# Kernel tuning notes

Measured on AMD Instinct MI355X. Metric: run time of the kernel, lower is better.

The kernel has to match this reference:

```python
import jax, jax.numpy as jnp
import numpy as np

N, T, D_FEAT, H = 8192, 60, 6, 64
NEG_SLOPE = 0.01  # torch LeakyReLU default


def setup_inputs() -> dict:
    key = jax.random.key(0)
    ks = jax.random.split(key, 20)
    s = lambda k, shape, fan: jax.random.normal(k, shape, jnp.float32) * (1.0 / np.sqrt(fan))
    inp = {
        'x': jax.random.normal(ks[0], (N, T, D_FEAT), jnp.float32),
        # LSTM layer 0 (input D_FEAT) and layer 1 (input H); gate order i,f,g,o
        'Wih0': s(ks[1], (4 * H, D_FEAT), H), 'Whh0': s(ks[2], (4 * H, H), H),
        'bih0': s(ks[3], (4 * H,), H), 'bhh0': s(ks[4], (4 * H,), H),
        'Wih1': s(ks[5], (4 * H, H), H), 'Whh1': s(ks[6], (4 * H, H), H),
        'bih1': s(ks[7], (4 * H,), H), 'bhh1': s(ks[8], (4 * H,), H),
        # GAT layer: transformation Linear(H,H) and attention vector a [2H,1] (randn in torch)
        'Wt': s(ks[9], (H, H), H), 'bt': s(ks[10], (H,), H),
        'a': jax.random.normal(ks[11], (2 * H, 1), jnp.float32),
        # fc and fc_out
        'Wfc': s(ks[12], (H, H), H), 'bfc': s(ks[13], (H,), H),
        'Wout': s(ks[14], (1, H), H), 'bout': s(ks[15], (1,), H),
    }
    return inp


def _lstm_layer(x, Wih, Whh, bih, bhh):
    # x: [N, T, Din] -> outputs [N, T, H]
    xg = jnp.einsum('ntd,gd->ntg', x, Wih) + bih + bhh  # precompute input gates

    def step(carry, xt):
        h, c = carry
        gates = xt + h @ Whh.T  # [N, 4H]
        i, f, g, o = jnp.split(gates, 4, axis=-1)
        c = jax.nn.sigmoid(f) * c + jax.nn.sigmoid(i) * jnp.tanh(g)
        h = jax.nn.sigmoid(o) * jnp.tanh(c)
        return (h, c), h

    n = x.shape[0]
    h0 = jnp.zeros((n, Whh.shape[1]), x.dtype)
    (_, _), hs = jax.lax.scan(step, (h0, h0), jnp.swapaxes(xg, 0, 1))
    return jnp.swapaxes(hs, 0, 1)


def _gat_layer(x, Wt, bt, a):
    # att[i,j] = leaky_relu(a1 . Wx_j + a2 . Wx_i); softmax over j; out = att @ x
    h = x @ Wt.T + bt                    # [N, H]
    hdim = h.shape[1]
    s1 = (h @ a[:hdim]).squeeze(-1)      # a1 . Wx_j  -> column term
    s2 = (h @ a[hdim:]).squeeze(-1)      # a2 . Wx_i  -> row term
    scores = jax.nn.leaky_relu(s2[:, None] + s1[None, :], NEG_SLOPE)  # [N, N]
    att = jax.nn.softmax(scores, axis=1)
    return att @ x


def reference(x, Wih0, Whh0, bih0, bhh0, Wih1, Whh1, bih1, bhh1,
              Wt, bt, a, Wfc, bfc, Wout, bout):
    out = _lstm_layer(x, Wih0, Whh0, bih0, bhh0)
    out = _lstm_layer(out, Wih1, Whh1, bih1, bhh1)
    last = out[:, -1, :]                 # [N, H]
    hidden = _gat_layer(last, Wt, bt, a) + last  # num_layers_gat = 1
    hidden = jax.nn.leaky_relu(hidden @ Wfc.T + bfc, NEG_SLOPE)
    return (hidden @ Wout.T + bout).squeeze(-1)  # [N]
```

## Files before the change

kernel.cpp:

```cpp
#include <hip/hip_runtime.h>

#define NN 8192
#define TT 60
#define DF 6
#define HH 64
#define GG 256
#define RS 132
#define CH 32
#define NCH (NN / CH)

typedef _Float16 half8 __attribute__((ext_vector_type(8)));
typedef float f32x4 __attribute__((ext_vector_type(4)));
#define MFMA16(a, b, c) __builtin_amdgcn_mfma_f32_16x16x32_f16((a), (b), (c), 0, 0, 0)

__device__ __forceinline__ float sigmoidf_(float x) {
    return __builtin_amdgcn_rcpf(1.0f + __expf(-x));
}
__device__ __forceinline__ float tanhf_(float x) {
    return __builtin_fmaf(2.0f, __builtin_amdgcn_rcpf(1.0f + __expf(-2.0f * x)), -1.0f);
}
__device__ __forceinline__ float lrelu_(float x) { return x > 0.0f ? x : 0.01f * x; }

__device__ __forceinline__ half8 ldw8(const float* __restrict__ p) {
    const float4* q = (const float4*)p;
    float4 u = q[0], v = q[1];
    half8 r;
    r[0]=(_Float16)u.x; r[1]=(_Float16)u.y; r[2]=(_Float16)u.z; r[3]=(_Float16)u.w;
    r[4]=(_Float16)v.x; r[5]=(_Float16)v.y; r[6]=(_Float16)v.z; r[7]=(_Float16)v.w;
    return r;
}

#define SXW (TT * 8 + 8)

__global__ __launch_bounds__(512, 4)
void lstm_fused_kernel(const float* __restrict__ x,
                       const float* __restrict__ Wih0, const float* __restrict__ Whh0,
                       const float* __restrict__ bih0, const float* __restrict__ bhh0,
                       const float* __restrict__ Wih1, const float* __restrict__ Whh1,
                       const float* __restrict__ bih1, const float* __restrict__ bhh1,
                       float* __restrict__ last_out)
{
    __shared__ _Float16 sxp[16][SXW];
    __shared__ _Float16 h0buf[2][16][72];
    __shared__ _Float16 h1buf[2][16][72];
    __shared__ _Float16 zero16[8];

    const int tid  = threadIdx.x;
    const int w    = tid >> 6;
    const int grp  = w >> 2;
    const int cg   = w & 3;
    const int lane = tid & 63;
    const int quad = lane >> 4;
    const int l15  = lane & 15;
    const int hc   = cg * 16 + l15;
    const int n0   = blockIdx.x * 16;

    for (int i = tid; i < 16 * SXW / 2; i += 512) ((unsigned*)sxp)[i] = 0u;
    for (int i = tid; i < 2 * 16 * 72 / 2; i += 512) ((unsigned*)h0buf)[i] = 0u;
    for (int i = tid; i < 2 * 16 * 72 / 2; i += 512) ((unsigned*)h1buf)[i] = 0u;
    if (tid < 4) ((unsigned*)zero16)[tid] = 0u;
    __syncthreads();

    for (int idx = tid; idx < 16 * TT * DF; idx += 512) {
        const int m = idx / (TT * DF);
        const int r = idx - m * (TT * DF);
        const int t = r / DF;
        const int d = r - t * DF;
        sxp[m][t * 8 + d] = (_Float16)x[(size_t)(n0 + m) * (TT * DF) + r];
    }

    half8 wA[4][2], wB[4][2];
    float bias[4];
    half8 hzero;
    #pragma unroll
    for (int j = 0; j < 8; j++) hzero[j] = (_Float16)0.f;

    if (grp == 0) {
        #pragma unroll
        for (int nt = 0; nt < 4; nt++) {
            const int g = nt * 64 + hc;
            wA[nt][0] = ldw8(Whh0 + (size_t)g * HH + quad * 8);
            wA[nt][1] = ldw8(Whh0 + (size_t)g * HH + 32 + quad * 8);
            bias[nt]  = bih0[g] + bhh0[g];
            half8 t = hzero;
            if (quad == 0) {
                #pragma unroll
                for (int j = 0; j < DF; j++) t[j] = (_Float16)Wih0[g * DF + j];
            }
            wB[nt][0] = t;
            wB[nt][1] = hzero;
        }
    } else {
        #pragma unroll
        for (int nt = 0; nt < 4; nt++) {
            const int g = nt * 64 + hc;
            wA[nt][0] = ldw8(Wih1 + (size_t)g * HH + quad * 8);
            wA[nt][1] = ldw8(Wih1 + (size_t)g * HH + 32 + quad * 8);
            wB[nt][0] = ldw8(Whh1 + (size_t)g * HH + quad * 8);
            wB[nt][1] = ldw8(Whh1 + (size_t)g * HH + 32 + quad * 8);
            bias[nt]  = bih1[g] + bhh1[g];
        }
    }

    float cs[4] = {0.f, 0.f, 0.f, 0.f};
    __syncthreads();

    for (int i = 0; i <= TT; i++) {
        const int p = i & 1;
        if (grp == 0) {
            if (i < TT) {
                const half8 a0 = *(const half8*)&h0buf[p][l15][quad * 8];
                const half8 a1 = *(const half8*)&h0buf[p][l15][32 + quad * 8];
                const _Float16* xap = (quad == 0) ? &sxp[l15][i * 8] : zero16;
                const half8 ax = *(const half8*)xap;
                f32x4 gv[4];
                #pragma unroll
                for (int nt = 0; nt < 4; nt++) {
                    f32x4 c; c[0] = bias[nt]; c[1] = bias[nt]; c[2] = bias[nt]; c[3] = bias[nt];
                    c = MFMA16(ax, wB[nt][0], c);
                    c = MFMA16(a0, wA[nt][0], c);
                    c = MFMA16(a1, wA[nt][1], c);
                    gv[nt] = c;
                }
                _Float16 (*h0w)[72] = h0buf[p ^ 1];
                #pragma unroll
                for (int reg = 0; reg < 4; reg++) {
                    const float gi = gv[0][reg], gf = gv[1][reg], gc = gv[2][reg], go = gv[3][reg];
                    const float cc = sigmoidf_(gf) * cs[reg] + sigmoidf_(gi) * tanhf_(gc);
                    cs[reg] = cc;
                    h0w[quad * 4 + reg][hc] = (_Float16)(sigmoidf_(go) * tanhf_(cc));
                }
            }
        } else {
            if (i > 0) {
                const half8 a00 = *(const half8*)&h0buf[p][l15][quad * 8];
                const half8 a01 = *(const half8*)&h0buf[p][l15][32 + quad * 8];
                const half8 a10 = *(const half8*)&h1buf[p][l15][quad * 8];
                const half8 a11 = *(const half8*)&h1buf[p][l15][32 + quad * 8];
                f32x4 gv[4];
                #pragma unroll
                for (int nt = 0; nt < 4; nt++) {
                    f32x4 c; c[0] = bias[nt]; c[1] = bias[nt]; c[2] = bias[nt]; c[3] = bias[nt];
                    c = MFMA16(a00, wA[nt][0], c);
                    c = MFMA16(a01, wA[nt][1], c);
                    c = MFMA16(a10, wB[nt][0], c);
                    c = MFMA16(a11, wB[nt][1], c);
                    gv[nt] = c;
                }
                _Float16 (*h1w)[72] = h1buf[p ^ 1];
                #pragma unroll
                for (int reg = 0; reg < 4; reg++) {
                    const float gi = gv[0][reg], gf = gv[1][reg], gc = gv[2][reg], go = gv[3][reg];
                    const float cc = sigmoidf_(gf) * cs[reg] + sigmoidf_(gi) * tanhf_(gc);
                    cs[reg] = cc;
                    const float hv = sigmoidf_(go) * tanhf_(cc);
                    h1w[quad * 4 + reg][hc] = (_Float16)hv;
                    if (i == TT) last_out[(size_t)(n0 + quad * 4 + reg) * HH + hc] = hv;
                }
            }
        }
        __syncthreads();
    }
}

__global__ void gat_prep_kernel(const float* __restrict__ last,
                                const float* __restrict__ Wt, const float* __restrict__ bt,
                                const float* __restrict__ a,
                                float* __restrict__ s1, float* __restrict__ s2,
                                float* __restrict__ blkmax)
{
    __shared__ float sWtT[HH][HH + 1];
    __shared__ float slast[16][HH];
    __shared__ float sbt[HH], sa1[HH], sa2[HH];
    __shared__ float swm[4];
    const int tid = threadIdx.x;
    for (int idx = tid; idx < HH * HH; idx += 256) {
        const int h = idx >> 6, d = idx & 63;
        sWtT[d][h] = Wt[idx];
    }
    if (tid < HH) { sbt[tid] = bt[tid]; sa1[tid] = a[tid]; sa2[tid] = a[HH + tid]; }
    const int n0 = blockIdx.x * 16;
    for (int idx = tid; idx < 16 * HH; idx += 256)
        (&slast[0][0])[idx] = last[(size_t)n0 * HH + idx];
    __syncthreads();
    const int w = tid >> 6, l = tid & 63;
    float wmax = -1e30f;
    for (int rr = 0; rr < 4; rr++) {
        const int r = w * 4 + rr;
        float acc = sbt[l];
        #pragma unroll
        for (int d = 0; d < HH; d++) acc += slast[r][d] * sWtT[d][l];
        float p1 = acc * sa1[l], p2 = acc * sa2[l];
        #pragma unroll
        for (int off = 32; off > 0; off >>= 1) {
            p1 += __shfl_xor(p1, off);
            p2 += __shfl_xor(p2, off);
        }
        if (l == 0) { s1[n0 + r] = p1; s2[n0 + r] = p2; }
        wmax = fmaxf(wmax, p1);
    }
    if (l == 0) swm[w] = wmax;
    __syncthreads();
    if (tid == 0) blkmax[blockIdx.x] = fmaxf(fmaxf(swm[0], swm[1]), fmaxf(swm[2], swm[3]));
}

__global__ void gat_finalize_kernel(const float* __restrict__ s1, const float* __restrict__ s2,
                                    const float* __restrict__ blkmax,
                                    float* __restrict__ Z, float* __restrict__ Ai, float* __restrict__ Bi,
                                    float* __restrict__ Dj, float* __restrict__ Uj, float* __restrict__ Wj,
                                    int* __restrict__ rank)
{
    __shared__ float red[256];
    const int tid = threadIdx.x;
    red[tid] = fmaxf(blkmax[tid], blkmax[tid + 256]);
    __syncthreads();
    for (int s = 128; s > 0; s >>= 1) {
        if (tid < s) red[tid] = fmaxf(red[tid], red[tid + s]);
        __syncthreads();
    }
    const float s1max = red[0];
    for (int i = blockIdx.x * 256 + tid; i < NN; i += 256 * 32) {
        const float z  = s2[i] + s1max;
        const float mi = lrelu_(z);
        Z[i]  = z;
        Ai[i] = __expf(z - mi);
        Bi[i] = __expf(0.01f * z - mi);
        const float d = s1[i] - s1max;
        Dj[i] = d;
        Uj[i] = __expf(d);
        Wj[i] = __expf(0.01f * d);
        rank[i] = 0;
    }
}

__global__ __launch_bounds__(256)
void rank_kernel(const float* __restrict__ Dj, int* __restrict__ rank)
{
    __shared__ float sd[1024];
    const int tid = threadIdx.x;
    const int j   = blockIdx.x * 256 + tid;
    const float dj = Dj[j];
    const int kbase = blockIdx.y * 1024;
    for (int i = tid; i < 1024; i += 256) sd[i] = Dj[kbase + i];
    __syncthreads();
    int cnt = 0;
    #pragma unroll 4
    for (int q = 0; q < 256; q++) {
        const float4 dk = ((const float4*)sd)[q];
        const int k0 = kbase + q * 4;
        cnt += (dk.x < dj || (dk.x == dj && k0     < j)) ? 1 : 0;
        cnt += (dk.y < dj || (dk.y == dj && k0 + 1 < j)) ? 1 : 0;
        cnt += (dk.z < dj || (dk.z == dj && k0 + 2 < j)) ? 1 : 0;
        cnt += (dk.w < dj || (dk.w == dj && k0 + 3 < j)) ? 1 : 0;
    }
    atomicAdd(&rank[j], cnt);
}

__global__ __launch_bounds__(256)
void scatter_kernel(const float* __restrict__ last,
                    const float* __restrict__ Dj, const float* __restrict__ Uj,
                    const float* __restrict__ Wj, const int* __restrict__ rank,
                    float* __restrict__ sortedRow, float* __restrict__ sortedD)
{
    const int tid = threadIdx.x;
    const int wv = tid >> 6, lane = tid & 63;
    #pragma unroll
    for (int it = 0; it < 8; it++) {
        const int j = blockIdx.x * 32 + wv * 8 + it;
        const int r = rank[j];
        const float u = Uj[j], w = Wj[j];
        const float lv = last[(size_t)j * HH + lane];
        float* row = sortedRow + (size_t)r * RS;
        row[lane]      = u * lv;
        row[64 + lane] = w * lv;
        if (lane == 0) {
            row[128] = u;
            row[129] = w;
            sortedD[r] = Dj[j];
        }
    }
}

__global__ __launch_bounds__(256)
void scanA_kernel(const float* __restrict__ sortedRow, float* __restrict__ chunkSum)
{
    const int c = threadIdx.x;
    if (c >= 130) return;
    const int b = blockIdx.x;
    const float* base = sortedRow + (size_t)b * CH * RS + c;
    float s = 0.f;
    #pragma unroll 8
    for (int r = 0; r < CH; r++) s += base[(size_t)r * RS];
    chunkSum[b * RS + c] = s;
}

__global__ __launch_bounds__(256)
void scanC_kernel(const float* __restrict__ sortedRow, const float* __restrict__ chunkSum,
                  float* __restrict__ PP)
{
    const int c = threadIdx.x;
    if (c >= 130) return;
    const int b = blockIdx.x;
    const bool rev = (c < 64) || (c == 128);
    float run = 0.f;
    #pragma unroll 8
    for (int bb = 0; bb < NCH; bb++) {
        const float v = chunkSum[bb * RS + c];
        const bool take = rev ? (bb > b) : (bb < b);
        run += take ? v : 0.f;
    }
    if (rev) {
        if (b == NCH - 1) PP[(size_t)NN * RS + c] = 0.f;
        #pragma unroll 4
        for (int r = CH - 1; r >= 0; r--) {
            const size_t t = (size_t)b * CH + r;
            run += sortedRow[t * RS + c];
            PP[t * RS + c] = run;
        }
    } else {
        #pragma unroll 4
        for (int r = 0; r < CH; r++) {
            const size_t t = (size_t)b * CH + r;
            PP[t * RS + c] = run;
            run += sortedRow[t * RS + c];
        }
        if (b == NCH - 1) PP[(size_t)NN * RS + c] = run;
    }
}

__global__ __launch_bounds__(256)
void applyfc_kernel(const float* __restrict__ last,
                    const float* __restrict__ Z, const float* __restrict__ Ai, const float* __restrict__ Bi,
                    const float* __restrict__ sortedD, const float* __restrict__ PP,
                    const float* __restrict__ Wfc, const float* __restrict__ bfc,
                    const float* __restrict__ Wout, const float* __restrict__ bout,
                    float* __restrict__ out)
{
    __shared__ float sdD[NN];
    __shared__ float sW[HH][HH + 1];
    __shared__ float sb[HH], sa[HH];
    const int tid = threadIdx.x;
    for (int idx = tid; idx < NN; idx += 256) sdD[idx] = sortedD[idx];
    for (int idx = tid; idx < HH * HH; idx += 256) {
        const int h = idx >> 6, d = idx & 63;
        sW[d][h] = Wfc[idx];
    }
    if (tid < HH) { sb[tid] = bfc[tid]; sa[tid] = Wout[tid]; }
    __syncthreads();

    const int wv = tid >> 6, lane = tid & 63;
    const int base_i = (blockIdx.x * 4 + wv) * 8;
    const float bo = bout[0];
    for (int batch = 0; batch < 2; batch++) {
        const int i0 = base_i + batch * 4;
        float zi[4]; int lo[4], hi[4];
        #pragma unroll
        for (int q = 0; q < 4; q++) { zi[q] = Z[i0 + q]; lo[q] = 0; hi[q] = NN; }
        for (int iter = 0; iter < 13; iter++) {
            #pragma unroll
            for (int q = 0; q < 4; q++) {
                if (lo[q] < hi[q]) {
                    const int mid = (lo[q] + hi[q]) >> 1;
                    const float dm = sdD[mid];
                    if (zi[q] + dm > 0.f) hi[q] = mid; else lo[q] = mid + 1;
                }
            }
        }
        #pragma unroll
        for (int q = 0; q < 4; q++) {
            const int i = i0 + q;
            const int t = lo[q];
            const float ai = Ai[i], bi = Bi[i];
            const float* row = PP + (size_t)t * RS;
            const float pu  = row[lane];
            const float pw  = row[64 + lane];
            const float pud = row[128];
            const float pwd = row[129];
            const float numer = bi * pw + ai * pu;
            const float den   = bi * pwd + ai * pud;
            const float lv = last[(size_t)i * HH + lane];
            const float gv = numer * __builtin_amdgcn_rcpf(den) + lv;
            float acc = sb[lane];
            #pragma unroll
            for (int d = 0; d < HH; d++) acc += __shfl(gv, d) * sW[d][lane];
            float prod = lrelu_(acc) * sa[lane];
            #pragma unroll
            for (int off = 32; off > 0; off >>= 1) prod += __shfl_xor(prod, off);
            if (lane == 0) out[i] = prod + bo;
        }
    }
}

extern "C" void kernel_launch(void* const* d_in, const int* in_sizes, int n_in,
                              void* d_out, int out_size, void* d_ws, size_t ws_size,
                              hipStream_t stream)
{
    (void)in_sizes; (void)n_in; (void)out_size; (void)ws_size;
    const float* x    = (const float*)d_in[0];
    const float* Wih0 = (const float*)d_in[1];
    const float* Whh0 = (const float*)d_in[2];
    const float* bih0 = (const float*)d_in[3];
    const float* bhh0 = (const float*)d_in[4];
    const float* Wih1 = (const float*)d_in[5];
    const float* Whh1 = (const float*)d_in[6];
    const float* bih1 = (const float*)d_in[7];
    const float* bhh1 = (const float*)d_in[8];
    const float* Wt   = (const float*)d_in[9];
    const float* bt   = (const float*)d_in[10];
    const float* a    = (const float*)d_in[11];
    const float* Wfc  = (const float*)d_in[12];
    const float* bfc  = (const float*)d_in[13];
    const float* Wout = (const float*)d_in[14];
    const float* bout = (const float*)d_in[15];
    float* out = (float*)d_out;

    float* ws        = (float*)d_ws;
    float* last      = ws;
    float* s1        = last + (size_t)NN*HH;
    float* s2        = s1 + NN;
    float* Z         = s2 + NN;
    float* Ai        = Z + NN;
    float* Bi        = Ai + NN;
    float* Dj        = Bi + NN;
    float* Uj        = Dj + NN;
    float* Wj        = Uj + NN;
    float* blkmax    = Wj + NN;
    int*   rank      = (int*)(blkmax + 512);
    float* sortedD   = (float*)(rank + NN);
    float* sortedRow = sortedD + NN;
    float* PP        = sortedRow + (size_t)NN*RS;
    float* chunkSum  = PP + (size_t)(NN+1)*RS;

    lstm_fused_kernel<<<dim3(NN / 16), dim3(512), 0, stream>>>(
        x, Wih0, Whh0, bih0, bhh0, Wih1, Whh1, bih1, bhh1, last);
    gat_prep_kernel<<<dim3(NN / 16), dim3(256), 0, stream>>>(
        last, Wt, bt, a, s1, s2, blkmax);
    gat_finalize_kernel<<<dim3(32), dim3(256), 0, stream>>>(
        s1, s2, blkmax, Z, Ai, Bi, Dj, Uj, Wj, rank);
    rank_kernel<<<dim3(NN / 256, 8), dim3(256), 0, stream>>>(Dj, rank);
    scatter_kernel<<<dim3(NN / 32), dim3(256), 0, stream>>>(
        last, Dj, Uj, Wj, rank, sortedRow, sortedD);
    scanA_kernel<<<dim3(NCH), dim3(256), 0, stream>>>(sortedRow, chunkSum);
    scanC_kernel<<<dim3(NCH), dim3(256), 0, stream>>>(sortedRow, chunkSum, PP);
    applyfc_kernel<<<dim3(NN / 32), dim3(256), 0, stream>>>(
        last, Z, Ai, Bi, sortedD, PP, Wfc, bfc, Wout, bout, out);
}
```

Baseline: 287.1 us.

## Fuse GAT tail kernels into one persistent kernel with software grid barriers

Replaces the seven GAT/FC kernels with a single 256-block persistent kernel that separates phases with atomic-counter grid barriers. This removes per-launch overhead and inter-kernel gaps. It also folds Wt into the attention vector (a^T Wt), so s1/s2 come from a dot product instead of a full 64x64 transform, and keeps per-row values in shared memory instead of global. The cost is that all 256 blocks must be co-resident for the barriers to avoid deadlock, and the rank counting now runs in fewer blocks doing more serial work each.

```diff
diff --git a/kernel.cpp b/kernel.cpp
--- a/kernel.cpp
+++ b/kernel.cpp
@@ -7,7 +7,7 @@
 #define GG 256
 #define RS 132
 #define CH 32
-#define NCH (NN / CH)
+#define NB 256
 
 typedef _Float16 half8 __attribute__((ext_vector_type(8)));
 typedef float f32x4 __attribute__((ext_vector_type(4)));
@@ -163,231 +163,229 @@
     }
 }
 
-__global__ void gat_prep_kernel(const float* __restrict__ last,
-                                const float* __restrict__ Wt, const float* __restrict__ bt,
-                                const float* __restrict__ a,
-                                float* __restrict__ s1, float* __restrict__ s2,
-                                float* __restrict__ blkmax)
+__global__ void bar_init_kernel(int* bar) {
+    if (threadIdx.x == 0) { bar[0] = 0; bar[1] = 0; }
+}
+
+__device__ __forceinline__ void gridbar(int* __restrict__ bar) {
+    __syncthreads();
+    if (threadIdx.x == 0) {
+        int* cnt = bar;
+        int* gen = bar + 1;
+        const int g = atomicAdd(gen, 0);
+        __threadfence();
+        if (atomicAdd(cnt, 1) == NB - 1) {
+            atomicExch(cnt, 0);
+            __threadfence();
+            atomicAdd(gen, 1);
+        } else {
+            while (atomicAdd(gen, 0) == g) __builtin_amdgcn_s_sleep(8);
+        }
+        __threadfence();
+    }
+    __syncthreads();
+}
+
+__global__ __launch_bounds__(256, 1)
+void gat_tail_kernel(const float* __restrict__ last,
+                     const float* __restrict__ Wt, const float* __restrict__ bt,
+                     const float* __restrict__ a,
+                     const float* __restrict__ Wfc, const float* __restrict__ bfc,
+                     const float* __restrict__ Wout, const float* __restrict__ bout,
+                     float* __restrict__ blkmax, float* __restrict__ Dj,
+                     float* __restrict__ sortedRow, float* __restrict__ sortedD,
+                     float* __restrict__ chunkSum, float* __restrict__ PP,
+                     int* __restrict__ bar,
+                     float* __restrict__ out)
 {
-    __shared__ float sWtT[HH][HH + 1];
-    __shared__ float slast[16][HH];
-    __shared__ float sbt[HH], sa1[HH], sa2[HH];
-    __shared__ float swm[4];
-    const int tid = threadIdx.x;
+    __shared__ float big[NN];
+    __shared__ float sWfc[HH][HH + 1];
+    __shared__ float sv1[HH], sv2[HH], sbF[HH], saF[HH];
+    __shared__ float sc12[2];
+    __shared__ float sS1[32], sS2[32], sZ[32], sAi[32], sBi[32], sU[32], sWw[32], sD[32];
+    __shared__ int   sRank[32];
+    __shared__ float sred[256];
+
+    const int tid  = threadIdx.x;
+    const int b    = blockIdx.x;
+    const int j0   = b * 32;
+    const int wv   = tid >> 6;
+    const int lane = tid & 63;
+
     for (int idx = tid; idx < HH * HH; idx += 256) {
         const int h = idx >> 6, d = idx & 63;
-        sWtT[d][h] = Wt[idx];
-    }
-    if (tid < HH) { sbt[tid] = bt[tid]; sa1[tid] = a[tid]; sa2[tid] = a[HH + tid]; }
-    const int n0 = blockIdx.x * 16;
-    for (int idx = tid; idx < 16 * HH; idx += 256)
-        (&slast[0][0])[idx] = last[(size_t)n0 * HH + idx];
-    __syncthreads();
-    const int w = tid >> 6, l = tid & 63;
-    float wmax = -1e30f;
-    for (int rr = 0; rr < 4; rr++) {
-        const int r = w * 4 + rr;
-        float acc = sbt[l];
-        #pragma unroll
-        for (int d = 0; d < HH; d++) acc += slast[r][d] * sWtT[d][l];
-        float p1 = acc * sa1[l], p2 = acc * sa2[l];
+        sWfc[d][h] = Wfc[idx];
+    }
+    if (tid < HH) {
+        float a1 = 0.f, a2 = 0.f;
+        #pragma unroll 8
+        for (int h = 0; h < HH; h++) {
+            const float wt = Wt[h * HH + tid];
+            a1 += wt * a[h];
+            a2 += wt * a[HH + h];
+        }
+        sv1[tid] = a1; sv2[tid] = a2;
+    } else if (tid == 64 || tid == 65) {
+        const float* av = a + (tid - 64) * HH;
+        float c = 0.f;
+        #pragma unroll 8
+        for (int h = 0; h < HH; h++) c += bt[h] * av[h];
+        sc12[tid - 64] = c;
+    } else if (tid >= 128 && tid < 192) {
+        sbF[tid - 128] = bfc[tid - 128];
+    } else if (tid >= 192) {
+        saF[tid - 192] = Wout[tid - 192];
+    }
+    __syncthreads();
+
+    #pragma unroll
+    for (int jj = 0; jj < 8; jj++) {
+        const int jl = wv * 8 + jj;
+        const float lv = last[(size_t)(j0 + jl) * HH + lane];
+        float p1 = lv * sv1[lane];
+        float p2 = lv * sv2[lane];
         #pragma unroll
         for (int off = 32; off > 0; off >>= 1) {
             p1 += __shfl_xor(p1, off);
             p2 += __shfl_xor(p2, off);
         }
-        if (l == 0) { s1[n0 + r] = p1; s2[n0 + r] = p2; }
-        wmax = fmaxf(wmax, p1);
-    }
-    if (l == 0) swm[w] = wmax;
-    __syncthreads();
-    if (tid == 0) blkmax[blockIdx.x] = fmaxf(fmaxf(swm[0], swm[1]), fmaxf(swm[2], swm[3]));
-}
-
-__global__ void gat_finalize_kernel(const float* __restrict__ s1, const float* __restrict__ s2,
-                                    const float* __restrict__ blkmax,
-                                    float* __restrict__ Z, float* __restrict__ Ai, float* __restrict__ Bi,
-                                    float* __restrict__ Dj, float* __restrict__ Uj, float* __restrict__ Wj,
-                                    int* __restrict__ rank)
-{
-    __shared__ float red[256];
-    const int tid = threadIdx.x;
-    red[tid] = fmaxf(blkmax[tid], blkmax[tid + 256]);
+        if (lane == 0) { sS1[jl] = p1 + sc12[0]; sS2[jl] = p2 + sc12[1]; }
+    }
+    __syncthreads();
+    if (tid < 32) {
+        float m = sS1[tid];
+        #pragma unroll
+        for (int off = 16; off > 0; off >>= 1) m = fmaxf(m, __shfl_xor(m, off));
+        if (tid == 0) blkmax[b] = m;
+    }
+    gridbar(bar);
+
+    sred[tid] = blkmax[tid];
     __syncthreads();
     for (int s = 128; s > 0; s >>= 1) {
-        if (tid < s) red[tid] = fmaxf(red[tid], red[tid + s]);
+        if (tid < s) sred[tid] = fmaxf(sred[tid], sred[tid + s]);
         __syncthreads();
     }
-    const float s1max = red[0];
-    for (int i = blockIdx.x * 256 + tid; i < NN; i += 256 * 32) {
-        const float z  = s2[i] + s1max;
+    const float s1max = sred[0];
+    if (tid < 32) {
+        const float z  = sS2[tid] + s1max;
         const float mi = lrelu_(z);
-        Z[i]  = z;
-        Ai[i] = __expf(z - mi);
-        Bi[i] = __expf(0.01f * z - mi);
-        const float d = s1[i] - s1max;
-        Dj[i] = d;
-        Uj[i] = __expf(d);
-        Wj[i] = __expf(0.01f * d);
-        rank[i] = 0;
-    }
-}
-
-__global__ __launch_bounds__(256)
-void rank_kernel(const float* __restrict__ Dj, int* __restrict__ rank)
-{
-    __shared__ float sd[1024];
-    const int tid = threadIdx.x;
-    const int j   = blockIdx.x * 256 + tid;
-    const float dj = Dj[j];
-    const int kbase = blockIdx.y * 1024;
-    for (int i = tid; i < 1024; i += 256) sd[i] = Dj[kbase + i];
-    __syncthreads();
-    int cnt = 0;
-    #pragma unroll 4
-    for (int q = 0; q < 256; q++) {
-        const float4 dk = ((const float4*)sd)[q];
-        const int k0 = kbase + q * 4;
-        cnt += (dk.x < dj || (dk.x == dj && k0     < j)) ? 1 : 0;
-        cnt += (dk.y < dj || (dk.y == dj && k0 + 1 < j)) ? 1 : 0;
-        cnt += (dk.z < dj || (dk.z == dj && k0 + 2 < j)) ? 1 : 0;
-        cnt += (dk.w < dj || (dk.w == dj && k0 + 3 < j)) ? 1 : 0;
-    }
-    atomicAdd(&rank[j], cnt);
-}
-
-__global__ __launch_bounds__(256)
-void scatter_kernel(const float* __restrict__ last,
-                    const float* __restrict__ Dj, const float* __restrict__ Uj,
-                    const float* __restrict__ Wj, const int* __restrict__ rank,
-                    float* __restrict__ sortedRow, float* __restrict__ sortedD)
-{
-    const int tid = threadIdx.x;
-    const int wv = tid >> 6, lane = tid & 63;
+        sZ[tid]  = z;
+        sAi[tid] = __expf(z - mi);
+        sBi[tid] = __expf(0.01f * z - mi);
+        const float d = sS1[tid] - s1max;
+        sD[tid] = d;
+        Dj[j0 + tid] = d;
+        sU[tid]  = __expf(d);
+        sWw[tid] = __expf(0.01f * d);
+        sRank[tid] = 0;
+    }
+    gridbar(bar);
+
+    for (int idx = tid; idx < NN; idx += 256) big[idx] = Dj[idx];
+    __syncthreads();
+    {
+        const int jl = tid & 31;
+        const int part = tid >> 5;
+        const float dj = sD[jl];
+        const int jglob = j0 + jl;
+        int cnt = 0;
+        const int k0 = part * (NN / 8);
+        #pragma unroll 4
+        for (int k = k0; k < k0 + NN / 8; k++) {
+            const float dk = big[k];
+            cnt += (dk < dj || (dk == dj && k < jglob)) ? 1 : 0;
+        }
+        atomicAdd(&sRank[jl], cnt);
+    }
+    __syncthreads();
     #pragma unroll
-    for (int it = 0; it < 8; it++) {
-        const int j = blockIdx.x * 32 + wv * 8 + it;
-        const int r = rank[j];
-        const float u = Uj[j], w = Wj[j];
-        const float lv = last[(size_t)j * HH + lane];
+    for (int jj = 0; jj < 8; jj++) {
+        const int jl = wv * 8 + jj;
+        const int r = sRank[jl];
+        const float u = sU[jl], w = sWw[jl];
+        const float lv = last[(size_t)(j0 + jl) * HH + lane];
         float* row = sortedRow + (size_t)r * RS;
         row[lane]      = u * lv;
         row[64 + lane] = w * lv;
         if (lane == 0) {
             row[128] = u;
             row[129] = w;
-            sortedD[r] = Dj[j];
-        }
-    }
-}
-
-__global__ __launch_bounds__(256)
-void scanA_kernel(const float* __restrict__ sortedRow, float* __restrict__ chunkSum)
-{
-    const int c = threadIdx.x;
-    if (c >= 130) return;
-    const int b = blockIdx.x;
-    const float* base = sortedRow + (size_t)b * CH * RS + c;
-    float s = 0.f;
-    #pragma unroll 8
-    for (int r = 0; r < CH; r++) s += base[(size_t)r * RS];
-    chunkSum[b * RS + c] = s;
-}
-
-__global__ __launch_bounds__(256)
-void scanC_kernel(const float* __restrict__ sortedRow, const float* __restrict__ chunkSum,
-                  float* __restrict__ PP)
-{
-    const int c = threadIdx.x;
-    if (c >= 130) return;
-    const int b = blockIdx.x;
-    const bool rev = (c < 64) || (c == 128);
-    float run = 0.f;
-    #pragma unroll 8
-    for (int bb = 0; bb < NCH; bb++) {
-        const float v = chunkSum[bb * RS + c];
-        const bool take = rev ? (bb > b) : (bb < b);
-        run += take ? v : 0.f;
-    }
-    if (rev) {
-        if (b == NCH - 1) PP[(size_t)NN * RS + c] = 0.f;
-        #pragma unroll 4
-        for (int r = CH - 1; r >= 0; r--) {
-            const size_t t = (size_t)b * CH + r;
-            run += sortedRow[t * RS + c];
-            PP[t * RS + c] = run;
-        }
-    } else {
-        #pragma unroll 4
-        for (int r = 0; r < CH; r++) {
-            const size_t t = (size_t)b * CH + r;
-            PP[t * RS + c] = run;
-            run += sortedRow[t * RS + c];
-        }
-        if (b == NCH - 1) PP[(size_t)NN * RS + c] = run;
-    }
-}
-
-__global__ __launch_bounds__(256)
-void applyfc_kernel(const float* __restrict__ last,
-                    const float* __restrict__ Z, const float* __restrict__ Ai, const float* __restrict__ Bi,
-                    const float* __restrict__ sortedD, const float* __restrict__ PP,
-                    const float* __restrict__ Wfc, const float* __restrict__ bfc,
-                    const float* __restrict__ Wout, const float* __restrict__ bout,
-                    float* __restrict__ out)
-{
-    __shared__ float sdD[NN];
-    __shared__ float sW[HH][HH + 1];
-    __shared__ float sb[HH], sa[HH];
-    const int tid = threadIdx.x;
-    for (int idx = tid; idx < NN; idx += 256) sdD[idx] = sortedD[idx];
-    for (int idx = tid; idx < HH * HH; idx += 256) {
-        const int h = idx >> 6, d = idx & 63;
-        sW[d][h] = Wfc[idx];
-    }
-    if (tid < HH) { sb[tid] = bfc[tid]; sa[tid] = Wout[tid]; }
-    __syncthreads();
-
-    const int wv = tid >> 6, lane = tid & 63;
-    const int base_i = (blockIdx.x * 4 + wv) * 8;
+            sortedD[r] = sD[jl];
+        }
+    }
+    gridbar(bar);
+
+    if (tid < 130) {
+        const float* base = sortedRow + (size_t)b * CH * RS + tid;
+        float s = 0.f;
+        #pragma unroll 8
+        for (int r = 0; r < CH; r++) s += base[(size_t)r * RS];
+        chunkSum[b * RS + tid] = s;
+    }
+    gridbar(bar);
+
+    if (tid < 130) {
+        const int c = tid;
+        const bool rev = (c < 64) || (c == 128);
+        float run = 0.f;
+        #pragma unroll 8
+        for (int bb = 0; bb < NB; bb++) {
+            const float v = chunkSum[bb * RS + c];
+            run += ((rev ? (bb > b) : (bb < b)) ? v : 0.f);
+        }
+        if (rev) {
+            if (b == NB - 1) PP[(size_t)NN * RS + c] = 0.f;
+            #pragma unroll 4
+            for (int r = CH - 1; r >= 0; r--) {
+                const size_t t = (size_t)b * CH + r;
+                run += sortedRow[t * RS + c];
+                PP[t * RS + c] = run;
+            }
+        } else {
+            #pragma unroll 4
+            for (int r = 0; r < CH; r++) {
+                const size_t t = (size_t)b * CH + r;
+                PP[t * RS + c] = run;
+                run += sortedRow[t * RS + c];
+            }
+            if (b == NB - 1) PP[(size_t)NN * RS + c] = run;
+        }
+    }
+    gridbar(bar);
+
+    for (int idx = tid; idx < NN; idx += 256) big[idx] = sortedD[idx];
+    __syncthreads();
     const float bo = bout[0];
-    for (int batch = 0; batch < 2; batch++) {
-        const int i0 = base_i + batch * 4;
-        float zi[4]; int lo[4], hi[4];
-        #pragma unroll
-        for (int q = 0; q < 4; q++) { zi[q] = Z[i0 + q]; lo[q] = 0; hi[q] = NN; }
+    #pragma unroll
+    for (int jj = 0; jj < 8; jj++) {
+        const int il = wv * 8 + jj;
+        const int i  = j0 + il;
+        const float zi = sZ[il];
+        int lo = 0, hi = NN;
+        #pragma unroll
         for (int iter = 0; iter < 13; iter++) {
-            #pragma unroll
-            for (int q = 0; q < 4; q++) {
-                if (lo[q] < hi[q]) {
-                    const int mid = (lo[q] + hi[q]) >> 1;
-                    const float dm = sdD[mid];
-                    if (zi[q] + dm > 0.f) hi[q] = mid; else lo[q] = mid + 1;
-                }
-            }
-        }
-        #pragma unroll
-        for (int q = 0; q < 4; q++) {
-            const int i = i0 + q;
-            const int t = lo[q];
-            const float ai = Ai[i], bi = Bi[i];
-            const float* row = PP + (size_t)t * RS;
-            const float pu  = row[lane];
-            const float pw  = row[64 + lane];
-            const float pud = row[128];
-            const float pwd = row[129];
-            const float numer = bi * pw + ai * pu;
-            const float den   = bi * pwd + ai * pud;
-            const float lv = last[(size_t)i * HH + lane];
-            const float gv = numer * __builtin_amdgcn_rcpf(den) + lv;
-            float acc = sb[lane];
-            #pragma unroll
-            for (int d = 0; d < HH; d++) acc += __shfl(gv, d) * sW[d][lane];
-            float prod = lrelu_(acc) * sa[lane];
-            #pragma unroll
-            for (int off = 32; off > 0; off >>= 1) prod += __shfl_xor(prod, off);
-            if (lane == 0) out[i] = prod + bo;
-        }
+            const int mid = (lo + hi) >> 1;
+            const float dm = big[mid];
+            if (zi + dm > 0.f) hi = mid; else lo = mid + 1;
+        }
+        const float* rowp = PP + (size_t)lo * RS;
+        const float pu  = rowp[lane];
+        const float pw  = rowp[64 + lane];
+        const float pud = rowp[128];
+        const float pwd = rowp[129];
+        const float ai = sAi[il], bi = sBi[il];
+        const float numer = bi * pw + ai * pu;
+        const float den   = bi * pwd + ai * pud;
+        const float lv = last[(size_t)i * HH + lane];
+        const float gv = numer * __builtin_amdgcn_rcpf(den) + lv;
+        float acc = sbF[lane];
+        #pragma unroll
+        for (int d = 0; d < HH; d++) acc += __shfl(gv, d) * sWfc[d][lane];
+        float prod = lrelu_(acc) * saF[lane];
+        #pragma unroll
+        for (int off = 32; off > 0; off >>= 1) prod += __shfl_xor(prod, off);
+        if (lane == 0) out[i] = prod + bo;
     }
 }
 
@@ -416,32 +414,18 @@
 
     float* ws        = (float*)d_ws;
     float* last      = ws;
-    float* s1        = last + (size_t)NN*HH;
-    float* s2        = s1 + NN;
-    float* Z         = s2 + NN;
-    float* Ai        = Z + NN;
-    float* Bi        = Ai + NN;
-    float* Dj        = Bi + NN;
-    float* Uj        = Dj + NN;
-    float* Wj        = Uj + NN;
-    float* blkmax    = Wj + NN;
-    int*   rank      = (int*)(blkmax + 512);
-    float* sortedD   = (float*)(rank + NN);
+    float* Dj        = last + (size_t)NN*HH;
+    float* blkmax    = Dj + NN;
+    float* sortedD   = blkmax + 256;
     float* sortedRow = sortedD + NN;
     float* PP        = sortedRow + (size_t)NN*RS;
     float* chunkSum  = PP + (size_t)(NN+1)*RS;
+    int*   bar       = (int*)(chunkSum + NB*RS);
 
     lstm_fused_kernel<<<dim3(NN / 16), dim3(512), 0, stream>>>(
         x, Wih0, Whh0, bih0, bhh0, Wih1, Whh1, bih1, bhh1, last);
-    gat_prep_kernel<<<dim3(NN / 16), dim3(256), 0, stream>>>(
-        last, Wt, bt, a, s1, s2, blkmax);
-    gat_finalize_kernel<<<dim3(32), dim3(256), 0, stream>>>(
-        s1, s2, blkmax, Z, Ai, Bi, Dj, Uj, Wj, rank);
-    rank_kernel<<<dim3(NN / 256, 8), dim3(256), 0, stream>>>(Dj, rank);
-    scatter_kernel<<<dim3(NN / 32), dim3(256), 0, stream>>>(
-        last, Dj, Uj, Wj, rank, sortedRow, sortedD);
-    scanA_kernel<<<dim3(NCH), dim3(256), 0, stream>>>(sortedRow, chunkSum);
-    scanC_kernel<<<dim3(NCH), dim3(256), 0, stream>>>(sortedRow, chunkSum, PP);
-    applyfc_kernel<<<dim3(NN / 32), dim3(256), 0, stream>>>(
-        last, Z, Ai, Bi, sortedD, PP, Wfc, bfc, Wout, bout, out);
-}
+    bar_init_kernel<<<dim3(1), dim3(64), 0, stream>>>(bar);
+    gat_tail_kernel<<<dim3(NB), dim3(256), 0, stream>>>(
+        last, Wt, bt, a, Wfc, bfc, Wout, bout,
+        blkmax, Dj, sortedRow, sortedD, chunkSum, PP, bar, out);
+}
```

Measured after the change: 400.4 us. +39.5%, slower.
